# Optimization experiments

Measured on AMD Instinct MI355X. Metric: run time of the kernel, lower is better.

Reference implementation:

```python
import jax, jax.numpy as jnp
import numpy as np

ALPHA = 0.2          # LeakyReLU negative slope
THRESHOLD = 0.5      # adjacency threshold
NEG_INF = -9e15      # same fill value as torch source


def setup_inputs() -> dict:
    key = jax.random.key(0)
    k_in, k_adj, k_W, k_a = jax.random.split(key, 4)
    B, N, C = 32, 1024, 64
    inp = jax.random.normal(k_in, (B, N, C), dtype=jnp.float32)
    adj = jax.random.uniform(k_adj, (N, N), dtype=jnp.float32)
    # xavier_uniform with gain=1.414 (as in torch init)
    gain = 1.414
    lim_W = gain * np.sqrt(6.0 / (C + C))
    W = jax.random.uniform(k_W, (C, C), dtype=jnp.float32, minval=-lim_W, maxval=lim_W)
    lim_a = gain * np.sqrt(6.0 / (2 * C + 1))
    a = jax.random.uniform(k_a, (2 * C, 1), dtype=jnp.float32, minval=-lim_a, maxval=lim_a)
    return {"input": inp, "adj": adj, "W": W, "a": a}


def reference(input, adj, W, a):
    # h: [B, N, C]
    h = jnp.matmul(input, W)
    C = W.shape[0]
    a_src = a[:C, 0]   # applied to h_i (row / query node)
    a_dst = a[C:, 0]   # applied to h_j (col / neighbor node)
    # Algebraic decomposition of a^T [h_i || h_j]: outer-sum of two [B,N] vectors.
    s_src = jnp.matmul(h, a_src)  # [B, N]
    s_dst = jnp.matmul(h, a_dst)  # [B, N]
    e = jax.nn.leaky_relu(s_src[:, :, None] + s_dst[:, None, :], negative_slope=ALPHA)  # [B,N,N]
    mask = adj > THRESHOLD  # [N, N], broadcast over batch
    attention = jax.nn.softmax(jnp.where(mask[None, :, :], e, NEG_INF), axis=2)
    h_prime = jnp.matmul(attention, h)  # [B, N, C]
    return jax.nn.elu(h_prime)
```

## Files before the change

kernel.cpp:

```cpp
#include <hip/hip_runtime.h>
#include <math.h>

#define ALPHA 0.2f

constexpr int B = 32, N = 1024, C = 64;
constexpr int TI = 16;
constexpr int TJ = 64;

typedef __attribute__((ext_vector_type(8))) short short8;
typedef __attribute__((ext_vector_type(4))) float floatx4;

static __device__ __forceinline__ unsigned f32bf(float f) {
    unsigned u = __float_as_uint(f);
    return (u + 0x7FFFu + ((u >> 16) & 1u)) >> 16;
}

__global__ __launch_bounds__(256) void gat_mask(const float* __restrict__ adj,
                                                const float* __restrict__ Wm,
                                                const float* __restrict__ a,
                                                unsigned long long* __restrict__ mask64,
                                                float* __restrict__ wa)
{
    const int lane = threadIdx.x & 63;
    const int wave = threadIdx.x >> 6;
    const int id   = blockIdx.x * 4 + wave;
    const int i    = id >> 4;
    const int jc   = id & 15;
    const float av = adj[(size_t)i * N + jc * 64 + lane];
    const unsigned long long bal = __ballot(av > 0.5f);
    if (lane == 0) mask64[i * 16 + jc] = bal;

    if (blockIdx.x == 0 && wave == 0) {
        float accs = 0.f, accd = 0.f;
#pragma unroll
        for (int c4 = 0; c4 < 16; ++c4) {
            const float4 wv = *(const float4*)&Wm[lane * 64 + c4 * 4];
            const float4 as = *(const float4*)&a[c4 * 4];
            const float4 ad = *(const float4*)&a[64 + c4 * 4];
            accs = fmaf(wv.x, as.x, fmaf(wv.y, as.y, fmaf(wv.z, as.z, fmaf(wv.w, as.w, accs))));
            accd = fmaf(wv.x, ad.x, fmaf(wv.y, ad.y, fmaf(wv.z, ad.z, fmaf(wv.w, ad.w, accd))));
        }
        wa[lane] = accs;
        wa[64 + lane] = accd;
    }
}

__global__ __launch_bounds__(256) void gat_hs(const float* __restrict__ input,
                                              const float* __restrict__ Wm,
                                              const float* __restrict__ wa,
                                              unsigned short* __restrict__ hT,
                                              float* __restrict__ ssrc,
                                              float* __restrict__ sdst)
{
    __shared__ __align__(16) float ins[64 * 68];
    __shared__ __align__(16) unsigned short hsT[64 * 72];
    __shared__ float red_s[256], red_d[256];
    __shared__ float wa_l[128];

    const int tid  = threadIdx.x;
    const int lane = tid & 63;
    const int wave = tid >> 6;
    const int row0 = blockIdx.x * 64;
    const int b    = row0 >> 10;
    const int jb   = row0 & 1023;

    float wreg[64];
#pragma unroll
    for (int k = 0; k < 64; ++k) wreg[k] = Wm[k * 64 + lane];

    const float4* gin = (const float4*)(input + (size_t)row0 * 64);
#pragma unroll
    for (int s = 0; s < 4; ++s) {
        const int id = tid + 256 * s;
        *(float4*)&ins[(id >> 4) * 68 + (id & 15) * 4] = gin[id];
    }
    if (tid < 128) wa_l[tid] = wa[tid];
    __syncthreads();

    for (int r = 0; r < 16; ++r) {
        const int row = wave * 16 + r;
        float acc = 0.f;
#pragma unroll
        for (int k4 = 0; k4 < 16; ++k4) {
            const float4 iv = *(const float4*)&ins[row * 68 + k4 * 4];
            acc = fmaf(iv.x, wreg[k4 * 4 + 0], acc);
            acc = fmaf(iv.y, wreg[k4 * 4 + 1], acc);
            acc = fmaf(iv.z, wreg[k4 * 4 + 2], acc);
            acc = fmaf(iv.w, wreg[k4 * 4 + 3], acc);
        }
        hsT[lane * 72 + row] = (unsigned short)f32bf(acc);
    }

    {
        const int r = tid & 63, kq = tid >> 6;
        float as = 0.f, ad = 0.f;
#pragma unroll
        for (int t = 0; t < 4; ++t) {
            const float4 iv = *(const float4*)&ins[r * 68 + kq * 16 + t * 4];
            const float4 ws = *(const float4*)&wa_l[kq * 16 + t * 4];
            const float4 wd = *(const float4*)&wa_l[64 + kq * 16 + t * 4];
            as = fmaf(iv.x, ws.x, fmaf(iv.y, ws.y, fmaf(iv.z, ws.z, fmaf(iv.w, ws.w, as))));
            ad = fmaf(iv.x, wd.x, fmaf(iv.y, wd.y, fmaf(iv.z, wd.z, fmaf(iv.w, wd.w, ad))));
        }
        red_s[tid] = as;
        red_d[tid] = ad;
    }
    __syncthreads();

    if (tid < 64) {
        ssrc[row0 + tid] = red_s[tid] + red_s[tid + 64] + red_s[tid + 128] + red_s[tid + 192];
        sdst[row0 + tid] = red_d[tid] + red_d[tid + 64] + red_d[tid + 128] + red_d[tid + 192];
    }

    {
        const int c = tid >> 2, part = tid & 3;
        const short8 v0 = *(const short8*)&hsT[c * 72 + part * 16];
        const short8 v1 = *(const short8*)&hsT[c * 72 + part * 16 + 8];
        const size_t g = ((size_t)(b * 64 + c)) * 1024 + jb + part * 16;
        *(short8*)&hT[g] = v0;
        *(short8*)&hT[g + 8] = v1;
    }
}

__global__ __launch_bounds__(256) void gat_attn(const unsigned short* __restrict__ hTg,
                                                const float* __restrict__ ssrc,
                                                const float* __restrict__ sdst,
                                                const unsigned* __restrict__ mask32,
                                                float* __restrict__ out)
{
    __shared__ __align__(16) unsigned short h_u[64 * 64];
    __shared__ __align__(16) unsigned short p_u[16 * 64];
    __shared__ float psum_s[16];

    const int tid  = threadIdx.x;
    const int lane = tid & 63;
    const int wave = tid >> 6;
    const int b    = blockIdx.x & 31;
    const int i0   = (blockIdx.x >> 5) * TI;

    const int ii = tid >> 4;
    const int jq = tid & 15;
    const float ssq = ssrc[b * N + i0 + ii];
    const unsigned short* hTb = hTg + (size_t)b * 64 * 1024;
    const float* sd = sdst + b * N;
    const unsigned* mrow = mask32 + (size_t)(i0 + ii) * 32;

    const int c = tid >> 2, m2 = tid & 3;
    const int hw0 = c * 64 + (((m2 * 2)    ) ^ (c & 7)) * 8;
    const int hw1 = c * 64 + (((m2 * 2 + 1)) ^ (c & 7)) * 8;
    const int pwi = ii * 64 + ((jq >> 1) ^ (ii & 7)) * 8 + (jq & 1) * 4;
    const int fa_ii = lane & 15, fq = lane >> 4;
    const int cB = wave * 16 + (lane & 15);

    floatx4 acc = {0.f, 0.f, 0.f, 0.f};
    float psacc = 0.f;

    for (int jt = 0; jt < 16; ++jt) {
        const short8 g0 = *(const short8*)&hTb[(size_t)c * 1024 + jt * 64 + m2 * 16];
        const short8 g1 = *(const short8*)&hTb[(size_t)c * 1024 + jt * 64 + m2 * 16 + 8];
        const float4 sd4 = *(const float4*)&sd[jt * 64 + jq * 4];
        const unsigned bits = mrow[jt * 2 + (jq >> 3)] >> ((jq & 7) * 4);

        __syncthreads();
        *(short8*)&h_u[hw0] = g0;
        *(short8*)&h_u[hw1] = g1;

        float e0 = ssq + sd4.x; e0 = e0 > 0.f ? e0 : ALPHA * e0;
        float e1 = ssq + sd4.y; e1 = e1 > 0.f ? e1 : ALPHA * e1;
        float e2 = ssq + sd4.z; e2 = e2 > 0.f ? e2 : ALPHA * e2;
        float e3 = ssq + sd4.w; e3 = e3 > 0.f ? e3 : ALPHA * e3;
        const float p0 = (bits & 1u) ? __expf(e0) : 0.f;
        const float p1 = (bits & 2u) ? __expf(e1) : 0.f;
        const float p2 = (bits & 4u) ? __expf(e2) : 0.f;
        const float p3 = (bits & 8u) ? __expf(e3) : 0.f;
        psacc += (p0 + p1) + (p2 + p3);
        const uint2 pw = {f32bf(p0) | (f32bf(p1) << 16), f32bf(p2) | (f32bf(p3) << 16)};
        *(uint2*)&p_u[pwi] = pw;
        __syncthreads();

#pragma unroll
        for (int t = 0; t < 2; ++t) {
            const short8 af = *(const short8*)&p_u[fa_ii * 64 + ((t * 4 + fq) ^ (fa_ii & 7)) * 8];
            const short8 bf = *(const short8*)&h_u[cB * 64 + ((t * 4 + fq) ^ (cB & 7)) * 8];
            acc = __builtin_amdgcn_mfma_f32_16x16x32_bf16(af, bf, acc, 0, 0, 0);
        }
    }

#pragma unroll
    for (int off = 1; off < 16; off <<= 1) psacc += __shfl_xor(psacc, off, 64);
    if ((tid & 15) == 0) psum_s[ii] = psacc;
    __syncthreads();

#pragma unroll
    for (int r = 0; r < 4; ++r) {
        const int row = fq * 4 + r;
        const float hp = acc[r] / psum_s[row];
        const float o = hp > 0.f ? hp : __expf(hp) - 1.f;
        out[((size_t)(b * N + i0 + row)) * 64 + wave * 16 + (lane & 15)] = o;
    }
}

extern "C" void kernel_launch(void* const* d_in, const int* in_sizes, int n_in,
                              void* d_out, int out_size, void* d_ws, size_t ws_size,
                              hipStream_t stream) {
    const float* input = (const float*)d_in[0];
    const float* adj   = (const float*)d_in[1];
    const float* Wm    = (const float*)d_in[2];
    const float* a     = (const float*)d_in[3];
    float* out = (float*)d_out;

    char* ws = (char*)d_ws;
    unsigned short* hT = (unsigned short*)ws;
    float* ssrc = (float*)(ws + 4194304);
    float* sdst = (float*)(ws + 4194304 + 131072);
    unsigned long long* mask64 = (unsigned long long*)(ws + 4194304 + 2 * 131072);
    float* wa = (float*)(ws + 4194304 + 3 * 131072);

    gat_mask<<<N * N / 64 / 4, 256, 0, stream>>>(adj, Wm, a, mask64, wa);
    gat_hs<<<B * N / 64, 256, 0, stream>>>(input, Wm, wa, hT, ssrc, sdst);
    gat_attn<<<(N / TI) * B, 256, 0, stream>>>(hT, ssrc, sdst, (const unsigned*)mask64, out);
}
```

Measured before the change: 96.83 us.

## Double-buffer P tile, load h fragments directly from global, double rows per block

The attention kernel now handles 32 query rows per block instead of 16, which halves the grid and reuses each B fragment across two MFMA accumulators. The h tile is no longer staged through LDS: each lane loads its MFMA B operand straight from global memory, and the next tile's loads are prefetched in registers. The probability tile is double-buffered in LDS, which drops to one barrier per iteration, and the exp computation for the next tile overlaps the current MFMAs. The trade-off is more register pressure and fewer blocks for occupancy, with uncoalesced 16-byte global loads per lane in place of cooperative staging.

```diff
diff --git a/kernel.cpp b/kernel.cpp
--- a/kernel.cpp
+++ b/kernel.cpp
@@ -4,8 +4,6 @@
 #define ALPHA 0.2f
 
 constexpr int B = 32, N = 1024, C = 64;
-constexpr int TI = 16;
-constexpr int TJ = 64;
 
 typedef __attribute__((ext_vector_type(8))) short short8;
 typedef __attribute__((ext_vector_type(4))) float floatx4;
@@ -125,78 +123,105 @@
 __global__ __launch_bounds__(256) void gat_attn(const unsigned short* __restrict__ hTg,
                                                 const float* __restrict__ ssrc,
                                                 const float* __restrict__ sdst,
-                                                const unsigned* __restrict__ mask32,
+                                                const unsigned char* __restrict__ maskB,
                                                 float* __restrict__ out)
 {
-    __shared__ __align__(16) unsigned short h_u[64 * 64];
-    __shared__ __align__(16) unsigned short p_u[16 * 64];
-    __shared__ float psum_s[16];
+    __shared__ __align__(16) unsigned short p_u[2][32 * 64];
+    __shared__ float psum_s[32];
 
     const int tid  = threadIdx.x;
     const int lane = tid & 63;
     const int wave = tid >> 6;
     const int b    = blockIdx.x & 31;
-    const int i0   = (blockIdx.x >> 5) * TI;
-
-    const int ii = tid >> 4;
-    const int jq = tid & 15;
+    const int i0   = (blockIdx.x >> 5) * 32;
+
+    const int ii = tid >> 3;
+    const int jo = tid & 7;
     const float ssq = ssrc[b * N + i0 + ii];
-    const unsigned short* hTb = hTg + (size_t)b * 64 * 1024;
-    const float* sd = sdst + b * N;
-    const unsigned* mrow = mask32 + (size_t)(i0 + ii) * 32;
-
-    const int c = tid >> 2, m2 = tid & 3;
-    const int hw0 = c * 64 + (((m2 * 2)    ) ^ (c & 7)) * 8;
-    const int hw1 = c * 64 + (((m2 * 2 + 1)) ^ (c & 7)) * 8;
-    const int pwi = ii * 64 + ((jq >> 1) ^ (ii & 7)) * 8 + (jq & 1) * 4;
-    const int fa_ii = lane & 15, fq = lane >> 4;
-    const int cB = wave * 16 + (lane & 15);
-
-    floatx4 acc = {0.f, 0.f, 0.f, 0.f};
+    const float* __restrict__ sd = sdst + b * N;
+    const unsigned char* __restrict__ mrow = maskB + (size_t)(i0 + ii) * 128;
+
+    const int n16 = lane & 15;
+    const int kq  = lane >> 4;
+    const int cB  = wave * 16 + n16;
+    const unsigned short* __restrict__ hTb = hTg + ((size_t)b * 64 + cB) * 1024;
+
+    const int pwoff = ii * 64 + (jo ^ (ii & 7)) * 8;
+    const int sw    = (n16 & 7);
+    const int ra0   = n16 * 64;
+    const int ra1   = (16 + n16) * 64;
+    const int ch0   = ((0 * 4 + kq) ^ sw) * 8;
+    const int ch1   = ((1 * 4 + kq) ^ sw) * 8;
+
+    floatx4 acc0 = {0.f, 0.f, 0.f, 0.f};
+    floatx4 acc1 = {0.f, 0.f, 0.f, 0.f};
     float psacc = 0.f;
 
+    auto compute_p = [&](int jt) -> short8 {
+        const float4 s0 = *(const float4*)&sd[jt * 64 + jo * 8];
+        const float4 s1 = *(const float4*)&sd[jt * 64 + jo * 8 + 4];
+        const unsigned mb = mrow[jt * 8 + jo];
+        const float ev[8] = {s0.x, s0.y, s0.z, s0.w, s1.x, s1.y, s1.z, s1.w};
+        short8 r;
+        float loc = 0.f;
+#pragma unroll
+        for (int k = 0; k < 8; ++k) {
+            float t = ssq + ev[k];
+            t = t > 0.f ? t : ALPHA * t;
+            const float p = ((mb >> k) & 1u) ? __expf(t) : 0.f;
+            loc += p;
+            r[k] = (short)f32bf(p);
+        }
+        psacc += loc;
+        return r;
+    };
+    auto load_B = [&](int jt, int t) -> short8 {
+        return *(const short8*)&hTb[jt * 64 + t * 32 + kq * 8];
+    };
+
+    short8 pk = compute_p(0);
+    short8 b0 = load_B(0, 0);
+    short8 b1 = load_B(0, 1);
+
     for (int jt = 0; jt < 16; ++jt) {
-        const short8 g0 = *(const short8*)&hTb[(size_t)c * 1024 + jt * 64 + m2 * 16];
-        const short8 g1 = *(const short8*)&hTb[(size_t)c * 1024 + jt * 64 + m2 * 16 + 8];
-        const float4 sd4 = *(const float4*)&sd[jt * 64 + jq * 4];
-        const unsigned bits = mrow[jt * 2 + (jq >> 3)] >> ((jq & 7) * 4);
-
+        unsigned short* pb = p_u[jt & 1];
+        *(short8*)&pb[pwoff] = pk;
         __syncthreads();
-        *(short8*)&h_u[hw0] = g0;
-        *(short8*)&h_u[hw1] = g1;
-
-        float e0 = ssq + sd4.x; e0 = e0 > 0.f ? e0 : ALPHA * e0;
-        float e1 = ssq + sd4.y; e1 = e1 > 0.f ? e1 : ALPHA * e1;
-        float e2 = ssq + sd4.z; e2 = e2 > 0.f ? e2 : ALPHA * e2;
-        float e3 = ssq + sd4.w; e3 = e3 > 0.f ? e3 : ALPHA * e3;
-        const float p0 = (bits & 1u) ? __expf(e0) : 0.f;
-        const float p1 = (bits & 2u) ? __expf(e1) : 0.f;
-        const float p2 = (bits & 4u) ? __expf(e2) : 0.f;
-        const float p3 = (bits & 8u) ? __expf(e3) : 0.f;
-        psacc += (p0 + p1) + (p2 + p3);
-        const uint2 pw = {f32bf(p0) | (f32bf(p1) << 16), f32bf(p2) | (f32bf(p3) << 16)};
-        *(uint2*)&p_u[pwi] = pw;
-        __syncthreads();
-
-#pragma unroll
-        for (int t = 0; t < 2; ++t) {
-            const short8 af = *(const short8*)&p_u[fa_ii * 64 + ((t * 4 + fq) ^ (fa_ii & 7)) * 8];
-            const short8 bf = *(const short8*)&h_u[cB * 64 + ((t * 4 + fq) ^ (cB & 7)) * 8];
-            acc = __builtin_amdgcn_mfma_f32_16x16x32_bf16(af, bf, acc, 0, 0, 0);
-        }
-    }
-
-#pragma unroll
-    for (int off = 1; off < 16; off <<= 1) psacc += __shfl_xor(psacc, off, 64);
-    if ((tid & 15) == 0) psum_s[ii] = psacc;
+
+        short8 nb0 = b0, nb1 = b1, npk = pk;
+        if (jt < 15) {
+            nb0 = load_B(jt + 1, 0);
+            nb1 = load_B(jt + 1, 1);
+            npk = compute_p(jt + 1);
+        }
+
+        const short8 a00 = *(const short8*)&pb[ra0 + ch0];
+        const short8 a01 = *(const short8*)&pb[ra0 + ch1];
+        const short8 a10 = *(const short8*)&pb[ra1 + ch0];
+        const short8 a11 = *(const short8*)&pb[ra1 + ch1];
+        acc0 = __builtin_amdgcn_mfma_f32_16x16x32_bf16(a00, b0, acc0, 0, 0, 0);
+        acc0 = __builtin_amdgcn_mfma_f32_16x16x32_bf16(a01, b1, acc0, 0, 0, 0);
+        acc1 = __builtin_amdgcn_mfma_f32_16x16x32_bf16(a10, b0, acc1, 0, 0, 0);
+        acc1 = __builtin_amdgcn_mfma_f32_16x16x32_bf16(a11, b1, acc1, 0, 0, 0);
+
+        b0 = nb0; b1 = nb1; pk = npk;
+    }
+
+#pragma unroll
+    for (int off = 1; off < 8; off <<= 1) psacc += __shfl_xor(psacc, off, 64);
+    if (jo == 0) psum_s[ii] = psacc;
     __syncthreads();
 
 #pragma unroll
-    for (int r = 0; r < 4; ++r) {
-        const int row = fq * 4 + r;
-        const float hp = acc[r] / psum_s[row];
-        const float o = hp > 0.f ? hp : __expf(hp) - 1.f;
-        out[((size_t)(b * N + i0 + row)) * 64 + wave * 16 + (lane & 15)] = o;
+    for (int it = 0; it < 2; ++it) {
+        const floatx4 acc = it ? acc1 : acc0;
+#pragma unroll
+        for (int r = 0; r < 4; ++r) {
+            const int row = it * 16 + kq * 4 + r;
+            const float hp = acc[r] / psum_s[row];
+            const float o  = hp > 0.f ? hp : __expf(hp) - 1.f;
+            out[((size_t)(b * N + i0 + row)) * 64 + cB] = o;
+        }
     }
 }
 
@@ -218,5 +243,5 @@
 
     gat_mask<<<N * N / 64 / 4, 256, 0, stream>>>(adj, Wm, a, mask64, wa);
     gat_hs<<<B * N / 64, 256, 0, stream>>>(input, Wm, wa, hT, ssrc, sdst);
-    gat_attn<<<(N / TI) * B, 256, 0, stream>>>(hT, ssrc, sdst, (const unsigned*)mask64, out);
-}
+    gat_attn<<<(N / 32) * B, 256, 0, stream>>>(hT, ssrc, sdst, (const unsigned char*)mask64, out);
+}
```

Result: slower. 105.4 us (+8.8%).
